# Optimization experiments

Measured on AMD Instinct MI355X. Metric: run time of the kernel, lower is better.

Reference implementation:

```python
import jax, jax.numpy as jnp
import numpy as np


def _windowed_attn(q, k, v, window_size, num_heads):
    # q, k, v: [B, T, D] with T % window_size == 0
    B, T, D = q.shape
    hd = D // num_heads
    scale = 1.0 / np.sqrt(hd).astype(np.float32)
    nw = T // window_size
    # [B, nw, w, H, hd]
    qh = q.reshape(B, nw, window_size, num_heads, hd)
    kh = k.reshape(B, nw, window_size, num_heads, hd)
    vh = v.reshape(B, nw, window_size, num_heads, hd)
    # attention scores per window: [B, nw, H, w, w]
    attn = jnp.einsum('bnqhd,bnkhd->bnhqk', qh, kh) * scale
    attn = jax.nn.softmax(attn, axis=-1)
    out = jnp.einsum('bnhqk,bnkhd->bnqhd', attn, vh)
    return out.reshape(B, T, D)


def setup_inputs() -> dict:
    key = jax.random.key(0)
    ks = jax.random.split(key, 6)
    B, D = 8, 512
    T1, T2 = 4096, 2048
    return {
        'q1': jax.random.normal(ks[0], (B, T1, D), dtype=jnp.float32),
        'k1': jax.random.normal(ks[1], (B, T1, D), dtype=jnp.float32),
        'v1': jax.random.normal(ks[2], (B, T1, D), dtype=jnp.float32),
        'q2': jax.random.normal(ks[3], (B, T2, D), dtype=jnp.float32),
        'k2': jax.random.normal(ks[4], (B, T2, D), dtype=jnp.float32),
        'v2': jax.random.normal(ks[5], (B, T2, D), dtype=jnp.float32),
        'window_size': 128,
        'num_heads': 8,
    }


def reference(q1, k1, v1, q2, k2, v2, window_size, num_heads):
    out1 = _windowed_attn(q1, k1, v1, window_size, num_heads)
    out2 = _windowed_attn(q2, k2, v2, window_size, num_heads)
    return (out1, out2)
```

## Files before the change

kernel.cpp:

```cpp
#include <hip/hip_runtime.h>
#include <hip/hip_bf16.h>

typedef __attribute__((ext_vector_type(4))) float f32x4;
typedef __attribute__((ext_vector_type(16))) float f32x16;
typedef __attribute__((ext_vector_type(8))) short bf16x8;

#define NH 8
#define HD 64
#define WSZ 128
#define DM 512

__device__ __forceinline__ unsigned int pk2bf(float lo, float hi) {
    union { __hip_bfloat162 h; unsigned int u; } r;
    r.h = __float22bfloat162_rn(make_float2(lo, hi));
    return r.u;
}

__device__ __forceinline__ bf16x8 pack8(f32x4 a, f32x4 b) {
    union { unsigned int u[4]; bf16x8 v; } r;
    r.u[0] = pk2bf(a[0], a[1]);
    r.u[1] = pk2bf(a[2], a[3]);
    r.u[2] = pk2bf(b[0], b[1]);
    r.u[3] = pk2bf(b[2], b[3]);
    return r.v;
}

__global__ __launch_bounds__(256, 4) void wattn_kernel(
    const float* __restrict__ q1, const float* __restrict__ k1,
    const float* __restrict__ v1, float* __restrict__ o1, int nw1,
    const float* __restrict__ q2, const float* __restrict__ k2,
    const float* __restrict__ v2, float* __restrict__ o2, int nw2,
    int nblk1)
{
    __shared__ __align__(16) unsigned short Kl[128 * 64];
    __shared__ __align__(16) unsigned short Vt[64 * 128];

    const int t = threadIdx.x;
    const int lane = t & 63;
    const int wid = t >> 6;
    const int hi = lane >> 5;
    const int c = lane & 31;

    int bid = blockIdx.x;
    const float *q, *k, *v; float* o; int nw;
    if (bid < nblk1) { q = q1; k = k1; v = v1; o = o1; nw = nw1; }
    else { bid -= nblk1; q = q2; k = k2; v = v2; o = o2; nw = nw2; }

    const int h = bid & (NH - 1);
    const int w = (bid / NH) % nw;
    const int b = bid / (NH * nw);

    const size_t row0 = ((size_t)b * nw + w) * WSZ;
    const float* Qp = q + row0 * DM + h * HD;
    const float* Kp = k + row0 * DM + h * HD;
    const float* Vp = v + row0 * DM + h * HD;
    float* Op = o + row0 * DM + h * HD;

#pragma unroll
    for (int i = 0; i < 4; ++i) {
        int row = i * 32 + (t >> 3);
        int colf = (t & 7) * 8;
        const float* src = Kp + (size_t)row * DM + colf;
        f32x4 a = *reinterpret_cast<const f32x4*>(src);
        f32x4 bq = *reinterpret_cast<const f32x4*>(src + 4);
        union { unsigned int u[4]; } wv;
        wv.u[0] = pk2bf(a[0], a[1]);  wv.u[1] = pk2bf(a[2], a[3]);
        wv.u[2] = pk2bf(bq[0], bq[1]); wv.u[3] = pk2bf(bq[2], bq[3]);
        *reinterpret_cast<unsigned int*>(&Kl[row * 64 + (colf ^ ((row & 7) << 3))]) = wv.u[0];
        *reinterpret_cast<unsigned int*>(&Kl[row * 64 + ((colf + 2) ^ ((row & 7) << 3))]) = wv.u[1];
        *reinterpret_cast<unsigned int*>(&Kl[row * 64 + ((colf + 4) ^ ((row & 7) << 3))]) = wv.u[2];
        *reinterpret_cast<unsigned int*>(&Kl[row * 64 + ((colf + 6) ^ ((row & 7) << 3))]) = wv.u[3];
    }

#pragma unroll
    for (int i = 0; i < 4; ++i) {
        int rp = i * 16 + (t >> 4);
        int dc = (t & 15) * 4;
        f32x4 va = *reinterpret_cast<const f32x4*>(Vp + (size_t)(2 * rp) * DM + dc);
        f32x4 vb = *reinterpret_cast<const f32x4*>(Vp + (size_t)(2 * rp + 1) * DM + dc);
#pragma unroll
        for (int j = 0; j < 4; ++j) {
            int d = dc + j;
            int idx = d * 128 + ((2 * rp) ^ (((d >> 1) & 7) << 3));
            *reinterpret_cast<unsigned int*>(&Vt[idx]) = pk2bf(va[j], vb[j]);
        }
    }

    const int qbase = wid * 32;
    bf16x8 qf[4];
#pragma unroll
    for (int ks = 0; ks < 4; ++ks) {
        const float* src = Qp + (size_t)(qbase + c) * DM + ks * 16 + hi * 8;
        f32x4 a = *reinterpret_cast<const f32x4*>(src);
        f32x4 bq = *reinterpret_cast<const f32x4*>(src + 4);
        qf[ks] = pack8(a, bq);
    }

    __syncthreads();

    f32x16 acc[4] = {};
#pragma unroll
    for (int ks = 0; ks < 4; ++ks) {
#pragma unroll
        for (int mf = 0; mf < 4; ++mf) {
            const bf16x8 kf = *reinterpret_cast<const bf16x8*>(
                &Kl[(mf * 32 + c) * 64 + ((ks * 16 + hi * 8) ^ ((c & 7) << 3))]);
            acc[mf] = __builtin_amdgcn_mfma_f32_32x32x16_bf16(kf, qf[ks], acc[mf], 0, 0, 0);
        }
    }

    const float CEXP = 0.125f * 1.4426950408889634f;
    float mx = acc[0][0];
#pragma unroll
    for (int f = 0; f < 4; ++f)
#pragma unroll
        for (int e = 0; e < 16; ++e) mx = fmaxf(mx, acc[f][e]);
    mx = fmaxf(mx, __shfl_xor(mx, 32));
    const float mxc = mx * CEXP;
    float sum = 0.f;
#pragma unroll
    for (int f = 0; f < 4; ++f)
#pragma unroll
        for (int e = 0; e < 16; ++e) {
            float p = exp2f(acc[f][e] * CEXP - mxc);
            acc[f][e] = p;
            sum += p;
        }
    sum += __shfl_xor(sum, 32);
    const float rinv = 1.0f / sum;

    f32x16 oacc[2] = {};
#pragma unroll
    for (int f = 0; f < 4; ++f) {
#pragma unroll
        for (int p = 0; p < 2; ++p) {
            const int kb = f * 2 + p;
            unsigned int U0 = pk2bf(acc[f][8 * p + 0], acc[f][8 * p + 1]);
            unsigned int U1 = pk2bf(acc[f][8 * p + 2], acc[f][8 * p + 3]);
            unsigned int U2 = pk2bf(acc[f][8 * p + 4], acc[f][8 * p + 5]);
            unsigned int U3 = pk2bf(acc[f][8 * p + 6], acc[f][8 * p + 7]);
            asm volatile("v_permlane32_swap_b32 %0, %1" : "+v"(U0), "+v"(U2));
            asm volatile("v_permlane32_swap_b32 %0, %1" : "+v"(U1), "+v"(U3));
            union { unsigned int u[4]; bf16x8 v; } A;
            A.u[0] = U0; A.u[1] = U1; A.u[2] = U2; A.u[3] = U3;
#pragma unroll
            for (int nf = 0; nf < 2; ++nf) {
                const int d = nf * 32 + c;
                const bf16x8 vf = *reinterpret_cast<const bf16x8*>(
                    &Vt[d * 128 + ((kb * 16 + hi * 8) ^ (((d >> 1) & 7) << 3))]);
                oacc[nf] = __builtin_amdgcn_mfma_f32_32x32x16_bf16(A.v, vf, oacc[nf], 0, 0, 0);
            }
        }
    }

#pragma unroll
    for (int reg = 0; reg < 16; ++reg) {
        const int qr = (reg & 3) + 8 * (reg >> 2) + 4 * hi;
        const float rv = __shfl(rinv, qr);
#pragma unroll
        for (int nf = 0; nf < 2; ++nf) {
            Op[(size_t)(qbase + qr) * DM + nf * 32 + c] = oacc[nf][reg] * rv;
        }
    }
}

extern "C" void kernel_launch(void* const* d_in, const int* in_sizes, int n_in,
                              void* d_out, int out_size, void* d_ws, size_t ws_size,
                              hipStream_t stream) {
    const float* q1 = (const float*)d_in[0];
    const float* k1 = (const float*)d_in[1];
    const float* v1 = (const float*)d_in[2];
    const float* q2 = (const float*)d_in[3];
    const float* k2 = (const float*)d_in[4];
    const float* v2 = (const float*)d_in[5];

    const int B = 8;
    const int nw1 = in_sizes[0] / (B * DM * WSZ);
    const int nw2 = in_sizes[3] / (B * DM * WSZ);

    float* o1 = (float*)d_out;
    float* o2 = o1 + (size_t)in_sizes[0];

    const int nblk1 = B * nw1 * NH;
    const int nblk2 = B * nw2 * NH;

    wattn_kernel<<<dim3(nblk1 + nblk2), dim3(256), 0, stream>>>(
        q1, k1, v1, o1, nw1, q2, k2, v2, o2, nw2, nblk1);
}
```

Measured before the change: 89.46 us.

## Make blocks persistent over tile chunks and prefetch next tile into registers

```diff
diff --git a/kernel.cpp b/kernel.cpp
--- a/kernel.cpp
+++ b/kernel.cpp
@@ -9,6 +9,8 @@
 #define HD 64
 #define WSZ 128
 #define DM 512
+#define CHUNK 6
+#define NTILE_TOTAL 3072
 
 __device__ __forceinline__ unsigned int pk2bf(float lo, float hi) {
     union { __hip_bfloat162 h; unsigned int u; } r;
@@ -25,12 +27,17 @@
     return r.v;
 }
 
-__global__ __launch_bounds__(256, 4) void wattn_kernel(
+__device__ __forceinline__ void lds_barrier() {
+    asm volatile("s_waitcnt lgkmcnt(0)" ::: "memory");
+    __builtin_amdgcn_s_barrier();
+}
+
+__global__ __launch_bounds__(256, 2) void wattn_kernel(
     const float* __restrict__ q1, const float* __restrict__ k1,
     const float* __restrict__ v1, float* __restrict__ o1, int nw1,
     const float* __restrict__ q2, const float* __restrict__ k2,
     const float* __restrict__ v2, float* __restrict__ o2, int nw2,
-    int nblk1)
+    int nt1)
 {
     __shared__ __align__(16) unsigned short Kl[128 * 64];
     __shared__ __align__(16) unsigned short Vt[64 * 128];
@@ -40,127 +47,158 @@
     const int wid = t >> 6;
     const int hi = lane >> 5;
     const int c = lane & 31;
-
-    int bid = blockIdx.x;
-    const float *q, *k, *v; float* o; int nw;
-    if (bid < nblk1) { q = q1; k = k1; v = v1; o = o1; nw = nw1; }
-    else { bid -= nblk1; q = q2; k = k2; v = v2; o = o2; nw = nw2; }
-
-    const int h = bid & (NH - 1);
-    const int w = (bid / NH) % nw;
-    const int b = bid / (NH * nw);
-
-    const size_t row0 = ((size_t)b * nw + w) * WSZ;
-    const float* Qp = q + row0 * DM + h * HD;
-    const float* Kp = k + row0 * DM + h * HD;
-    const float* Vp = v + row0 * DM + h * HD;
-    float* Op = o + row0 * DM + h * HD;
-
-#pragma unroll
-    for (int i = 0; i < 4; ++i) {
-        int row = i * 32 + (t >> 3);
-        int colf = (t & 7) * 8;
-        const float* src = Kp + (size_t)row * DM + colf;
-        f32x4 a = *reinterpret_cast<const f32x4*>(src);
-        f32x4 bq = *reinterpret_cast<const f32x4*>(src + 4);
-        union { unsigned int u[4]; } wv;
-        wv.u[0] = pk2bf(a[0], a[1]);  wv.u[1] = pk2bf(a[2], a[3]);
-        wv.u[2] = pk2bf(bq[0], bq[1]); wv.u[3] = pk2bf(bq[2], bq[3]);
-        *reinterpret_cast<unsigned int*>(&Kl[row * 64 + (colf ^ ((row & 7) << 3))]) = wv.u[0];
-        *reinterpret_cast<unsigned int*>(&Kl[row * 64 + ((colf + 2) ^ ((row & 7) << 3))]) = wv.u[1];
-        *reinterpret_cast<unsigned int*>(&Kl[row * 64 + ((colf + 4) ^ ((row & 7) << 3))]) = wv.u[2];
-        *reinterpret_cast<unsigned int*>(&Kl[row * 64 + ((colf + 6) ^ ((row & 7) << 3))]) = wv.u[3];
-    }
-
-#pragma unroll
-    for (int i = 0; i < 4; ++i) {
-        int rp = i * 16 + (t >> 4);
-        int dc = (t & 15) * 4;
-        f32x4 va = *reinterpret_cast<const f32x4*>(Vp + (size_t)(2 * rp) * DM + dc);
-        f32x4 vb = *reinterpret_cast<const f32x4*>(Vp + (size_t)(2 * rp + 1) * DM + dc);
-#pragma unroll
-        for (int j = 0; j < 4; ++j) {
-            int d = dc + j;
-            int idx = d * 128 + ((2 * rp) ^ (((d >> 1) & 7) << 3));
-            *reinterpret_cast<unsigned int*>(&Vt[idx]) = pk2bf(va[j], vb[j]);
-        }
-    }
-
     const int qbase = wid * 32;
-    bf16x8 qf[4];
-#pragma unroll
-    for (int ks = 0; ks < 4; ++ks) {
-        const float* src = Qp + (size_t)(qbase + c) * DM + ks * 16 + hi * 8;
-        f32x4 a = *reinterpret_cast<const f32x4*>(src);
-        f32x4 bq = *reinterpret_cast<const f32x4*>(src + 4);
-        qf[ks] = pack8(a, bq);
-    }
-
-    __syncthreads();
-
-    f32x16 acc[4] = {};
-#pragma unroll
-    for (int ks = 0; ks < 4; ++ks) {
-#pragma unroll
-        for (int mf = 0; mf < 4; ++mf) {
-            const bf16x8 kf = *reinterpret_cast<const bf16x8*>(
-                &Kl[(mf * 32 + c) * 64 + ((ks * 16 + hi * 8) ^ ((c & 7) << 3))]);
-            acc[mf] = __builtin_amdgcn_mfma_f32_32x32x16_bf16(kf, qf[ks], acc[mf], 0, 0, 0);
-        }
-    }
-
-    const float CEXP = 0.125f * 1.4426950408889634f;
-    float mx = acc[0][0];
-#pragma unroll
-    for (int f = 0; f < 4; ++f)
-#pragma unroll
-        for (int e = 0; e < 16; ++e) mx = fmaxf(mx, acc[f][e]);
-    mx = fmaxf(mx, __shfl_xor(mx, 32));
-    const float mxc = mx * CEXP;
-    float sum = 0.f;
-#pragma unroll
-    for (int f = 0; f < 4; ++f)
+
+    f32x4 ka[4], kb[4], va[4], vb[4], qa[4], qb[4];
+
+    auto tile_ptrs = [&](int ti, const float*& Qp, const float*& Kp,
+                         const float*& Vp, float*& Op) {
+        const float *q, *k, *v; float* o; int nw; int widx = ti;
+        if (widx < nt1) { q = q1; k = k1; v = v1; o = o1; nw = nw1; }
+        else { widx -= nt1; q = q2; k = k2; v = v2; o = o2; nw = nw2; }
+        const int h = widx & (NH - 1);
+        const int w = (widx / NH) % nw;
+        const int b = (widx / NH) / nw;
+        const size_t row0 = ((size_t)b * nw + w) * WSZ;
+        Qp = q + row0 * DM + h * HD;
+        Kp = k + row0 * DM + h * HD;
+        Vp = v + row0 * DM + h * HD;
+        Op = o + row0 * DM + h * HD;
+    };
+
+    auto issue = [&](const float* Qp, const float* Kp, const float* Vp) {
+#pragma unroll
+        for (int i = 0; i < 4; ++i) {
+            int row = i * 32 + (t >> 3);
+            const float* src = Kp + (size_t)row * DM + (t & 7) * 8;
+            ka[i] = *reinterpret_cast<const f32x4*>(src);
+            kb[i] = *reinterpret_cast<const f32x4*>(src + 4);
+        }
+#pragma unroll
+        for (int i = 0; i < 4; ++i) {
+            int rp = i * 16 + (t >> 4);
+            int dc = (t & 15) * 4;
+            va[i] = *reinterpret_cast<const f32x4*>(Vp + (size_t)(2 * rp) * DM + dc);
+            vb[i] = *reinterpret_cast<const f32x4*>(Vp + (size_t)(2 * rp + 1) * DM + dc);
+        }
+#pragma unroll
+        for (int ks = 0; ks < 4; ++ks) {
+            const float* src = Qp + (size_t)(qbase + c) * DM + ks * 16 + hi * 8;
+            qa[ks] = *reinterpret_cast<const f32x4*>(src);
+            qb[ks] = *reinterpret_cast<const f32x4*>(src + 4);
+        }
+    };
+
+    const int ti0 = blockIdx.x * CHUNK;
+    const float *Qp, *Kp, *Vp; float* Op;
+    tile_ptrs(ti0, Qp, Kp, Vp, Op);
+    issue(Qp, Kp, Vp);
+
+    for (int j = 0; j < CHUNK; ++j) {
+#pragma unroll
+        for (int i = 0; i < 4; ++i) {
+            int row = i * 32 + (t >> 3);
+            int colf = (t & 7) * 8;
+            int base = row * 64, sw = (row & 7) << 3;
+            *reinterpret_cast<unsigned int*>(&Kl[base + (colf ^ sw)]) = pk2bf(ka[i][0], ka[i][1]);
+            *reinterpret_cast<unsigned int*>(&Kl[base + ((colf + 2) ^ sw)]) = pk2bf(ka[i][2], ka[i][3]);
+            *reinterpret_cast<unsigned int*>(&Kl[base + ((colf + 4) ^ sw)]) = pk2bf(kb[i][0], kb[i][1]);
+            *reinterpret_cast<unsigned int*>(&Kl[base + ((colf + 6) ^ sw)]) = pk2bf(kb[i][2], kb[i][3]);
+        }
+#pragma unroll
+        for (int i = 0; i < 4; ++i) {
+            int rp = i * 16 + (t >> 4);
+            int dc = (t & 15) * 4;
+#pragma unroll
+            for (int jj = 0; jj < 4; ++jj) {
+                int d = dc + jj;
+                *reinterpret_cast<unsigned int*>(
+                    &Vt[d * 128 + ((2 * rp) ^ (((d >> 1) & 7) << 3))]) = pk2bf(va[i][jj], vb[i][jj]);
+            }
+        }
+        bf16x8 qf[4];
+#pragma unroll
+        for (int ks = 0; ks < 4; ++ks) qf[ks] = pack8(qa[ks], qb[ks]);
+
+        lds_barrier();
+
+        float* OpStore = Op;
+        if (j + 1 < CHUNK) {
+            tile_ptrs(ti0 + j + 1, Qp, Kp, Vp, Op);
+            issue(Qp, Kp, Vp);
+        }
+
+        f32x16 acc[4] = {};
+#pragma unroll
+        for (int ks = 0; ks < 4; ++ks) {
+#pragma unroll
+            for (int mf = 0; mf < 4; ++mf) {
+                const bf16x8 kf = *reinterpret_cast<const bf16x8*>(
+                    &Kl[(mf * 32 + c) * 64 + ((ks * 16 + hi * 8) ^ ((c & 7) << 3))]);
+                acc[mf] = __builtin_amdgcn_mfma_f32_32x32x16_bf16(kf, qf[ks], acc[mf], 0, 0, 0);
+            }
+        }
+
+        const float CEXP = 0.125f * 1.4426950408889634f;
+        float mxa = fmaxf(acc[0][0], acc[1][0]);
+        float mxb = fmaxf(acc[2][0], acc[3][0]);
+#pragma unroll
+        for (int e = 1; e < 16; ++e) {
+            mxa = fmaxf(mxa, fmaxf(acc[0][e], acc[1][e]));
+            mxb = fmaxf(mxb, fmaxf(acc[2][e], acc[3][e]));
+        }
+        float mx = fmaxf(mxa, mxb);
+        mx = fmaxf(mx, __shfl_xor(mx, 32));
+        const float mxc = mx * CEXP;
+        float s0 = 0.f, s1 = 0.f, s2 = 0.f, s3 = 0.f;
 #pragma unroll
         for (int e = 0; e < 16; ++e) {
-            float p = exp2f(acc[f][e] * CEXP - mxc);
-            acc[f][e] = p;
-            sum += p;
-        }
-    sum += __shfl_xor(sum, 32);
-    const float rinv = 1.0f / sum;
-
-    f32x16 oacc[2] = {};
-#pragma unroll
-    for (int f = 0; f < 4; ++f) {
-#pragma unroll
-        for (int p = 0; p < 2; ++p) {
-            const int kb = f * 2 + p;
-            unsigned int U0 = pk2bf(acc[f][8 * p + 0], acc[f][8 * p + 1]);
-            unsigned int U1 = pk2bf(acc[f][8 * p + 2], acc[f][8 * p + 3]);
-            unsigned int U2 = pk2bf(acc[f][8 * p + 4], acc[f][8 * p + 5]);
-            unsigned int U3 = pk2bf(acc[f][8 * p + 6], acc[f][8 * p + 7]);
-            asm volatile("v_permlane32_swap_b32 %0, %1" : "+v"(U0), "+v"(U2));
-            asm volatile("v_permlane32_swap_b32 %0, %1" : "+v"(U1), "+v"(U3));
-            union { unsigned int u[4]; bf16x8 v; } A;
-            A.u[0] = U0; A.u[1] = U1; A.u[2] = U2; A.u[3] = U3;
+            float p0 = exp2f(acc[0][e] * CEXP - mxc);
+            float p1 = exp2f(acc[1][e] * CEXP - mxc);
+            float p2 = exp2f(acc[2][e] * CEXP - mxc);
+            float p3 = exp2f(acc[3][e] * CEXP - mxc);
+            acc[0][e] = p0; acc[1][e] = p1; acc[2][e] = p2; acc[3][e] = p3;
+            s0 += p0; s1 += p1; s2 += p2; s3 += p3;
+        }
+        float sum = (s0 + s1) + (s2 + s3);
+        sum += __shfl_xor(sum, 32);
+        const float rinv = 1.0f / sum;
+
+        f32x16 oacc[2] = {};
+#pragma unroll
+        for (int f = 0; f < 4; ++f) {
+#pragma unroll
+            for (int p = 0; p < 2; ++p) {
+                const int kb2 = f * 2 + p;
+                unsigned int U0 = pk2bf(acc[f][8 * p + 0], acc[f][8 * p + 1]);
+                unsigned int U1 = pk2bf(acc[f][8 * p + 2], acc[f][8 * p + 3]);
+                unsigned int U2 = pk2bf(acc[f][8 * p + 4], acc[f][8 * p + 5]);
+                unsigned int U3 = pk2bf(acc[f][8 * p + 6], acc[f][8 * p + 7]);
+                asm volatile("v_permlane32_swap_b32 %0, %1" : "+v"(U0), "+v"(U2));
+                asm volatile("v_permlane32_swap_b32 %0, %1" : "+v"(U1), "+v"(U3));
+                union { unsigned int u[4]; bf16x8 v; } A;
+                A.u[0] = U0; A.u[1] = U1; A.u[2] = U2; A.u[3] = U3;
+#pragma unroll
+                for (int nf = 0; nf < 2; ++nf) {
+                    const int d = nf * 32 + c;
+                    const bf16x8 vf = *reinterpret_cast<const bf16x8*>(
+                        &Vt[d * 128 + ((kb2 * 16 + hi * 8) ^ (((d >> 1) & 7) << 3))]);
+                    oacc[nf] = __builtin_amdgcn_mfma_f32_32x32x16_bf16(A.v, vf, oacc[nf], 0, 0, 0);
+                }
+            }
+        }
+
+#pragma unroll
+        for (int reg = 0; reg < 16; ++reg) {
+            const int qr = (reg & 3) + 8 * (reg >> 2) + 4 * hi;
+            const float rv = __shfl(rinv, qr);
 #pragma unroll
             for (int nf = 0; nf < 2; ++nf) {
-                const int d = nf * 32 + c;
-                const bf16x8 vf = *reinterpret_cast<const bf16x8*>(
-                    &Vt[d * 128 + ((kb * 16 + hi * 8) ^ (((d >> 1) & 7) << 3))]);
-                oacc[nf] = __builtin_amdgcn_mfma_f32_32x32x16_bf16(A.v, vf, oacc[nf], 0, 0, 0);
-            }
-        }
-    }
-
-#pragma unroll
-    for (int reg = 0; reg < 16; ++reg) {
-        const int qr = (reg & 3) + 8 * (reg >> 2) + 4 * hi;
-        const float rv = __shfl(rinv, qr);
-#pragma unroll
-        for (int nf = 0; nf < 2; ++nf) {
-            Op[(size_t)(qbase + qr) * DM + nf * 32 + c] = oacc[nf][reg] * rv;
-        }
+                OpStore[(size_t)(qbase + qr) * DM + nf * 32 + c] = oacc[nf][reg] * rv;
+            }
+        }
+
+        lds_barrier();
     }
 }
 
@@ -181,9 +219,10 @@
     float* o1 = (float*)d_out;
     float* o2 = o1 + (size_t)in_sizes[0];
 
-    const int nblk1 = B * nw1 * NH;
-    const int nblk2 = B * nw2 * NH;
-
-    wattn_kernel<<<dim3(nblk1 + nblk2), dim3(256), 0, stream>>>(
-        q1, k1, v1, o1, nw1, q2, k2, v2, o2, nw2, nblk1);
-}
+    const int nt1 = B * nw1 * NH;
+    const int nt2 = B * nw2 * NH;
+    const int nblk = (nt1 + nt2) / CHUNK;
+
+    wattn_kernel<<<dim3(nblk), dim3(256), 0, stream>>>(
+        q1, k1, v1, o1, nw1, q2, k2, v2, o2, nw2, nt1);
+}
```

Result: slower. 101.5 us (+13.5%).
